# Performance work log

Measured on AMD Instinct MI355X. Metric: run time of the kernel, lower is better.

The kernel has to match this reference:

```python
import jax, jax.numpy as jnp
import numpy as np

B = 4096      # batch
F = 26        # num sparse features
L = 10        # pooling factor (multi-hot indices per feature)
V = 100000    # rows per embedding table
D = 128       # embedding dim (== dense_arch_layer_sizes[-1])
DENSE_IN = 13
DENSE_SIZES = [512, 256, 128]
OVER_SIZES = [1024, 1024, 512, 256, 1]
OVER_IN = D + (F * (F - 1)) // 2 + F  # 479


def _linear_params(key, dims, prefix):
    out = {}
    ks = jax.random.split(key, len(dims) - 1)
    for i in range(len(dims) - 1):
        fan_in = dims[i]
        out[f"{prefix}W{i}"] = jax.random.normal(ks[i], (dims[i], dims[i + 1]), jnp.float32) / np.sqrt(fan_in)
        out[f"{prefix}b{i}"] = jnp.zeros((dims[i + 1],), jnp.float32)
    return out


def setup_inputs() -> dict:
    key = jax.random.key(0)
    k0, k1, k2, k3, k4 = jax.random.split(key, 5)
    inp = {
        "dense_features": jax.random.normal(k0, (B, DENSE_IN), jnp.float32),
        "indices": jax.random.randint(k1, (B, F, L), 0, V, dtype=jnp.int64),
        "tables": jax.random.normal(k2, (F, V, D), jnp.float32) * 0.01,
    }
    inp.update(_linear_params(k3, [DENSE_IN] + DENSE_SIZES, "d"))
    inp.update(_linear_params(k4, [OVER_IN] + OVER_SIZES, "o"))
    return inp


def _dlrm_forward(dense_features, indices, tables,
                  dW0, db0, dW1, db1, dW2, db2,
                  oW0, ob0, oW1, ob1, oW2, ob2, oW3, ob3, oW4, ob4):
    b = dense_features.shape[0]
    # DenseArch: MLP with relu on every layer
    x = dense_features
    for W, bb in ((dW0, db0), (dW1, db1), (dW2, db2)):
        x = jax.nn.relu(x @ W + bb)
    embedded_dense = x  # [B, D]

    # SparseArch: pooled (sum) embedding lookup per feature -> [B, F, D]
    flat_tables = tables.reshape(F * V, D)
    offs = jnp.arange(F, dtype=indices.dtype) * V
    flat_idx = (indices + offs[None, :, None]).reshape(-1)
    gathered = jnp.take(flat_tables, flat_idx, axis=0).reshape(b, F, L, D)
    embedded_sparse = gathered.sum(axis=2)  # [B, F, D]

    # InteractionArch: bmm + upper-triangular gather
    z = jnp.concatenate([embedded_dense[:, None, :], embedded_sparse], axis=1)  # [B, F+1, D]
    inter = jnp.einsum("bnd,bmd->bnm", z, z)  # [B, F+1, F+1]
    iu0, iu1 = np.triu_indices(F + 1, k=1)
    inter_flat = inter[:, iu0, iu1]  # [B, C(F+1,2)]
    feats = jnp.concatenate([embedded_dense, inter_flat], axis=1)  # [B, OVER_IN]

    # OverArch: relu MLP on layer_sizes[:-1], then plain final Linear
    y = feats
    for W, bb in ((oW0, ob0), (oW1, ob1), (oW2, ob2), (oW3, ob3)):
        y = jax.nn.relu(y @ W + bb)
    logits = y @ oW4 + ob4  # [B, 1]
    return logits


def reference(dense_features, indices, tables,
              dW0, db0, dW1, db1, dW2, db2,
              oW0, ob0, oW1, ob1, oW2, ob2, oW3, ob3, oW4, ob4):
    return _dlrm_forward(dense_features, indices, tables,
                         dW0, db0, dW1, db1, dW2, db2,
                         oW0, ob0, oW1, ob1, oW2, ob2, oW3, ob3, oW4, ob4)
```

## Files before the change

kernel.cpp:

```cpp
#include <hip/hip_runtime.h>

#define B_ 4096
#define F_ 26
#define L_ 10
#define V_ 100000
#define D_ 128

typedef __attribute__((ext_vector_type(8))) short short8;
typedef __attribute__((ext_vector_type(4))) float f32x4;

__device__ inline unsigned pack_split(float f) {
    union { float f; unsigned u; } a; a.f = f;
    unsigned r = (a.u + 0x7FFFu + ((a.u >> 16) & 1u)) >> 16;
    union { unsigned u; float f; } hf; hf.u = r << 16;
    float rem = f - hf.f;
    union { float f; unsigned u; } b; b.f = rem;
    unsigned r2 = (b.u + 0x7FFFu + ((b.u >> 16) & 1u)) >> 16;
    return (r << 16) | (r2 & 0xFFFFu);
}
__device__ inline float unpack_f(unsigned u) {
    union { unsigned u; float f; } h; h.u = u & 0xFFFF0000u;
    union { unsigned u; float f; } l; l.u = u << 16;
    return h.f + l.f;
}

__device__ void prep_tile(const float* __restrict__ W, unsigned* __restrict__ Wt,
                          int K, int N, int Kp, int local)
{
    __shared__ float tile[32][33];
    const int t = threadIdx.x;
    const int tx = t & 31, ty = t >> 5;
    const int nbt = N >> 5;
    const int nb = (local % nbt) << 5, kb = (local / nbt) << 5;
    #pragma unroll
    for (int i = 0; i < 4; ++i) {
        int k = kb + ty + i * 8;
        tile[ty + i * 8][tx] = (k < K) ? W[(size_t)k * N + nb + tx] : 0.f;
    }
    __syncthreads();
    #pragma unroll
    for (int i = 0; i < 4; ++i) {
        int nl = ty + i * 8;
        Wt[(size_t)(nb + nl) * Kp + kb + tx] = pack_split(tile[tx][nl]);
    }
}

__global__ __launch_bounds__(256) void prep_all(
    const float* dW0, const float* dW1, const float* dW2,
    const float* oW0, const float* oW1, const float* oW2, const float* oW3,
    unsigned* dWt0, unsigned* dWt1, unsigned* dWt2,
    unsigned* oWt0, unsigned* oWt1, unsigned* oWt2, unsigned* oWt3,
    const float* dense, unsigned* densep)
{
    const int bid = blockIdx.x;
    if      (bid < 16)   prep_tile(dW0, dWt0, 13,   512,  32,   bid);
    else if (bid < 144)  prep_tile(dW1, dWt1, 512,  256,  512,  bid - 16);
    else if (bid < 176)  prep_tile(dW2, dWt2, 256,  128,  256,  bid - 144);
    else if (bid < 656)  prep_tile(oW0, oWt0, 479,  1024, 480,  bid - 176);
    else if (bid < 1680) prep_tile(oW1, oWt1, 1024, 1024, 1024, bid - 656);
    else if (bid < 2192) prep_tile(oW2, oWt2, 1024, 512,  1024, bid - 1680);
    else if (bid < 2320) prep_tile(oW3, oWt3, 512,  256,  512,  bid - 2192);
    else {
        int g = (bid - 2320) * 256 + threadIdx.x;
        int b = g >> 5, k = g & 31;
        densep[g] = (k < 13) ? pack_split(dense[(size_t)b * 13 + k]) : 0u;
    }
}

template<bool RELU>
__global__ __launch_bounds__(256) void gemm_db(
    const unsigned* __restrict__ Ap, const unsigned* __restrict__ Wt,
    const float* __restrict__ bias, unsigned* __restrict__ Cp,
    int M, int N, int Kp)
{
    __shared__ __align__(16) unsigned Au[2][128 * 32];
    __shared__ __align__(16) unsigned Bu[2][128 * 32];

    const int t    = threadIdx.x;
    const int lane = t & 63;
    const int w    = t >> 6;
    const int wm   = w >> 1, wn = w & 1;
    const int m0   = blockIdx.y * 128, n0 = blockIdx.x * 128;

    f32x4 acc[4][4];
    const f32x4 zero = {0.f, 0.f, 0.f, 0.f};
    #pragma unroll
    for (int i = 0; i < 4; ++i)
        #pragma unroll
        for (int j = 0; j < 4; ++j) acc[i][j] = zero;

    const unsigned* Ab = Ap + (size_t)m0 * Kp;
    const unsigned* Bb = Wt + (size_t)n0 * Kp;

    const int g4 = lane >> 4;
    const int rr = lane & 15;

    auto STAGE = [&](int buf, int k0) {
        #pragma unroll
        for (int i = 0; i < 4; ++i) {
            int chunk = t + (i << 8);
            int row = chunk >> 3, ch = chunk & 7;
            int sch = ch ^ (row & 7);
            __builtin_amdgcn_global_load_lds(
                (const __attribute__((address_space(1))) unsigned*)(Ab + (size_t)row * Kp + k0 + (sch << 2)),
                &Au[buf][chunk << 2], 16, 0, 0);
            __builtin_amdgcn_global_load_lds(
                (const __attribute__((address_space(1))) unsigned*)(Bb + (size_t)row * Kp + k0 + (sch << 2)),
                &Bu[buf][chunk << 2], 16, 0, 0);
        }
    };

    auto COMPUTE = [&](int buf) {
        const unsigned* au = Au[buf];
        const unsigned* bu = Bu[buf];
        short8 bh[4], bl[4];
        #pragma unroll
        for (int tj = 0; tj < 4; ++tj) {
            int r = wn * 64 + tj * 16 + rr;
            int c0 = (2 * g4) ^ (r & 7), c1 = (2 * g4 + 1) ^ (r & 7);
            uint4 p = *reinterpret_cast<const uint4*>(&bu[r * 32 + (c0 << 2)]);
            uint4 q = *reinterpret_cast<const uint4*>(&bu[r * 32 + (c1 << 2)]);
            union { short8 s; uint4 u; } H, L;
            H.u.x = __builtin_amdgcn_perm(p.y, p.x, 0x07060302u);
            L.u.x = __builtin_amdgcn_perm(p.y, p.x, 0x05040100u);
            H.u.y = __builtin_amdgcn_perm(p.w, p.z, 0x07060302u);
            L.u.y = __builtin_amdgcn_perm(p.w, p.z, 0x05040100u);
            H.u.z = __builtin_amdgcn_perm(q.y, q.x, 0x07060302u);
            L.u.z = __builtin_amdgcn_perm(q.y, q.x, 0x05040100u);
            H.u.w = __builtin_amdgcn_perm(q.w, q.z, 0x07060302u);
            L.u.w = __builtin_amdgcn_perm(q.w, q.z, 0x05040100u);
            bh[tj] = H.s; bl[tj] = L.s;
        }
        #pragma unroll
        for (int ti = 0; ti < 4; ++ti) {
            int r = wm * 64 + ti * 16 + rr;
            int c0 = (2 * g4) ^ (r & 7), c1 = (2 * g4 + 1) ^ (r & 7);
            uint4 p = *reinterpret_cast<const uint4*>(&au[r * 32 + (c0 << 2)]);
            uint4 q = *reinterpret_cast<const uint4*>(&au[r * 32 + (c1 << 2)]);
            union { short8 s; uint4 u; } H, L;
            H.u.x = __builtin_amdgcn_perm(p.y, p.x, 0x07060302u);
            L.u.x = __builtin_amdgcn_perm(p.y, p.x, 0x05040100u);
            H.u.y = __builtin_amdgcn_perm(p.w, p.z, 0x07060302u);
            L.u.y = __builtin_amdgcn_perm(p.w, p.z, 0x05040100u);
            H.u.z = __builtin_amdgcn_perm(q.y, q.x, 0x07060302u);
            L.u.z = __builtin_amdgcn_perm(q.y, q.x, 0x05040100u);
            H.u.w = __builtin_amdgcn_perm(q.w, q.z, 0x07060302u);
            L.u.w = __builtin_amdgcn_perm(q.w, q.z, 0x05040100u);
            short8 ah = H.s, al = L.s;
            #pragma unroll
            for (int tj = 0; tj < 4; ++tj) {
                f32x4 c = acc[ti][tj];
                c = __builtin_amdgcn_mfma_f32_16x16x32_bf16(ah, bh[tj], c, 0, 0, 0);
                c = __builtin_amdgcn_mfma_f32_16x16x32_bf16(ah, bl[tj], c, 0, 0, 0);
                c = __builtin_amdgcn_mfma_f32_16x16x32_bf16(al, bh[tj], c, 0, 0, 0);
                acc[ti][tj] = c;
            }
        }
    };

    const int nt = Kp >> 5;
    STAGE(0, 0);
    __syncthreads();
    int cur = 0;
    for (int ts = 0; ts < nt - 1; ++ts) {
        STAGE(cur ^ 1, (ts + 1) << 5);
        COMPUTE(cur);
        __syncthreads();
        cur ^= 1;
    }
    COMPUTE(cur);

    #pragma unroll
    for (int ti = 0; ti < 4; ++ti) {
        int row = m0 + wm * 64 + ti * 16 + ((lane >> 4) << 2);
        #pragma unroll
        for (int tj = 0; tj < 4; ++tj) {
            int col = n0 + wn * 64 + tj * 16 + (lane & 15);
            float bv = bias[col];
            #pragma unroll
            for (int r = 0; r < 4; ++r) {
                float v = acc[ti][tj][r] + bv;
                if (RELU) v = fmaxf(v, 0.f);
                Cp[(size_t)(row + r) * N + col] = pack_split(v);
            }
        }
    }
}

__global__ __launch_bounds__(256) void gather_interact(
    const unsigned* __restrict__ x2p,
    const int*      __restrict__ idx_words,
    const float*    __restrict__ tables,
    unsigned*       __restrict__ featsp)
{
    __shared__ __align__(16) float z[27][132];
    __shared__ int sidx[F_ * L_];
    __shared__ int sstride;
    const int b = blockIdx.x;
    const int t = threadIdx.x;

    if (t == 0) {
        int st = 2;
        for (int ww = 1; ww < 256; ww += 2)
            if (idx_words[ww] != 0) { st = 1; break; }
        sstride = st;
        featsp[(size_t)b * 480 + 479] = 0u;
    }
    __syncthreads();
    const int st = sstride;

    for (int s = t; s < F_ * L_; s += 256) {
        int v = idx_words[((size_t)b * F_ * L_ + s) * st];
        sidx[s] = v < 0 ? 0 : (v >= V_ ? V_ - 1 : v);
    }
    if (t < 128) {
        unsigned u = x2p[(size_t)b * 128 + t];
        z[0][t] = unpack_f(u);
        featsp[(size_t)b * 480 + t] = u;
    }
    __syncthreads();

    for (int s = t; s < F_ * 32; s += 256) {
        int f = s >> 5, d4 = s & 31;
        const float* tab = tables + (size_t)f * V_ * D_;
        float4 a4 = {0.f, 0.f, 0.f, 0.f};
        #pragma unroll
        for (int l = 0; l < L_; ++l) {
            int idx = sidx[f * L_ + l];
            float4 v = *reinterpret_cast<const float4*>(tab + (size_t)idx * D_ + (d4 << 2));
            a4.x += v.x; a4.y += v.y; a4.z += v.z; a4.w += v.w;
        }
        *reinterpret_cast<float4*>(&z[f + 1][d4 << 2]) = a4;
    }
    __syncthreads();

    for (int p = t; p < 351; p += 256) {
        int i = 0, rem = p;
        while (rem >= 26 - i) { rem -= 26 - i; ++i; }
        int j = i + 1 + rem;
        float4 s4 = {0.f, 0.f, 0.f, 0.f};
        for (int kk = 0; kk < 32; ++kk) {
            int k4 = (kk + t) & 31;
            float4 a = *reinterpret_cast<const float4*>(&z[i][k4 << 2]);
            float4 c = *reinterpret_cast<const float4*>(&z[j][k4 << 2]);
            s4.x += a.x * c.x; s4.y += a.y * c.y; s4.z += a.z * c.z; s4.w += a.w * c.w;
        }
        featsp[(size_t)b * 480 + 128 + p] = pack_split(s4.x + s4.y + s4.z + s4.w);
    }
}

__global__ __launch_bounds__(256) void final_dot(
    const unsigned* __restrict__ yp, const float* __restrict__ w,
    const float* __restrict__ bias, float* __restrict__ out)
{
    const int wave = threadIdx.x >> 6;
    const int lane = threadIdx.x & 63;
    const int b = blockIdx.x * 4 + wave;
    uint4 u = *reinterpret_cast<const uint4*>(yp + (size_t)b * 256 + lane * 4);
    float4 wv = *reinterpret_cast<const float4*>(&w[lane * 4]);
    float s = unpack_f(u.x) * wv.x + unpack_f(u.y) * wv.y +
              unpack_f(u.z) * wv.z + unpack_f(u.w) * wv.w;
    #pragma unroll
    for (int off = 32; off; off >>= 1) s += __shfl_xor(s, off);
    if (lane == 0) out[b] = s + bias[0];
}

extern "C" void kernel_launch(void* const* d_in, const int* in_sizes, int n_in,
                              void* d_out, int out_size, void* d_ws, size_t ws_size,
                              hipStream_t stream)
{
    const float* dense   = (const float*)d_in[0];
    const int*   indices = (const int*)  d_in[1];
    const float* tables  = (const float*)d_in[2];
    const float* dW0 = (const float*)d_in[3];  const float* db0 = (const float*)d_in[4];
    const float* dW1 = (const float*)d_in[5];  const float* db1 = (const float*)d_in[6];
    const float* dW2 = (const float*)d_in[7];  const float* db2 = (const float*)d_in[8];
    const float* oW0 = (const float*)d_in[9];  const float* ob0 = (const float*)d_in[10];
    const float* oW1 = (const float*)d_in[11]; const float* ob1 = (const float*)d_in[12];
    const float* oW2 = (const float*)d_in[13]; const float* ob2 = (const float*)d_in[14];
    const float* oW3 = (const float*)d_in[15]; const float* ob3 = (const float*)d_in[16];
    const float* oW4 = (const float*)d_in[17]; const float* ob4 = (const float*)d_in[18];
    float* out = (float*)d_out;

    unsigned* wsu = (unsigned*)d_ws;
    unsigned* dWt0 = wsu + 0;
    unsigned* dWt1 = wsu + 16384;
    unsigned* dWt2 = wsu + 147456;
    unsigned* oWt0 = wsu + 180224;
    unsigned* oWt1 = wsu + 671744;
    unsigned* oWt2 = wsu + 1720320;
    unsigned* oWt3 = wsu + 2244608;
    unsigned* densep = wsu + 2375680;
    unsigned* x2p    = wsu + 2506752;
    unsigned* featsp = wsu + 3031040;
    unsigned* x0p    = wsu + 5000000;
    unsigned* x1p    = wsu + 7097152;
    unsigned* y0p    = wsu + 5000000;
    unsigned* y1p    = wsu + 9194304;
    unsigned* y2p    = wsu + 2506752;
    unsigned* y3p    = wsu + 5000000;

    prep_all<<<2832, 256, 0, stream>>>(dW0, dW1, dW2, oW0, oW1, oW2, oW3,
                                       dWt0, dWt1, dWt2, oWt0, oWt1, oWt2, oWt3,
                                       dense, densep);

    gemm_db<true><<<dim3(4, B_ / 128), 256, 0, stream>>>(densep, dWt0, db0, x0p, B_, 512, 32);
    gemm_db<true><<<dim3(2, B_ / 128), 256, 0, stream>>>(x0p,    dWt1, db1, x1p, B_, 256, 512);
    gemm_db<true><<<dim3(1, B_ / 128), 256, 0, stream>>>(x1p,    dWt2, db2, x2p, B_, 128, 256);

    gather_interact<<<B_, 256, 0, stream>>>(x2p, indices, tables, featsp);

    gemm_db<true><<<dim3(8, B_ / 128), 256, 0, stream>>>(featsp, oWt0, ob0, y0p, B_, 1024, 480);
    gemm_db<true><<<dim3(8, B_ / 128), 256, 0, stream>>>(y0p,    oWt1, ob1, y1p, B_, 1024, 1024);
    gemm_db<true><<<dim3(4, B_ / 128), 256, 0, stream>>>(y1p,    oWt2, ob2, y2p, B_, 512, 1024);
    gemm_db<true><<<dim3(2, B_ / 128), 256, 0, stream>>>(y2p,    oWt3, ob3, y3p, B_, 256, 512);

    final_dot<<<B_ / 4, 256, 0, stream>>>(y3p, oW4, ob4, out);
}
```

Baseline: 327.2 us.

## Use 8-wave GEMM blocks and MFMA-based per-sample interaction with wave-per-sample gather

The GEMM kernel now runs 512 threads (8 waves) per 128x128 tile, so each wave owns a 64x32 sub-tile and keeps fewer accumulators, which is meant to raise latency hiding without changing the tile size. The embedding gather and interaction kernel is restructured so each wave handles one sample. The pooled embeddings are split into bf16 hi/lo halves in swizzled LDS, and the 27x27 Gram matrix is computed with split-bf16 MFMA instead of scalar float dot products. This removes the scalar triangular loop and shrinks the grid, at the cost of computing the full padded 32x32 product and using fewer threads per gather.

```diff
diff --git a/kernel.cpp b/kernel.cpp
--- a/kernel.cpp
+++ b/kernel.cpp
@@ -68,7 +68,7 @@
 }
 
 template<bool RELU>
-__global__ __launch_bounds__(256) void gemm_db(
+__global__ __launch_bounds__(512) void gemm8(
     const unsigned* __restrict__ Ap, const unsigned* __restrict__ Wt,
     const float* __restrict__ bias, unsigned* __restrict__ Cp,
     int M, int N, int Kp)
@@ -79,15 +79,15 @@
     const int t    = threadIdx.x;
     const int lane = t & 63;
     const int w    = t >> 6;
-    const int wm   = w >> 1, wn = w & 1;
+    const int wm   = w >> 2, wn = w & 3;
     const int m0   = blockIdx.y * 128, n0 = blockIdx.x * 128;
 
-    f32x4 acc[4][4];
+    f32x4 acc[4][2];
     const f32x4 zero = {0.f, 0.f, 0.f, 0.f};
     #pragma unroll
     for (int i = 0; i < 4; ++i)
         #pragma unroll
-        for (int j = 0; j < 4; ++j) acc[i][j] = zero;
+        for (int j = 0; j < 2; ++j) acc[i][j] = zero;
 
     const unsigned* Ab = Ap + (size_t)m0 * Kp;
     const unsigned* Bb = Wt + (size_t)n0 * Kp;
@@ -97,13 +97,19 @@
 
     auto STAGE = [&](int buf, int k0) {
         #pragma unroll
-        for (int i = 0; i < 4; ++i) {
-            int chunk = t + (i << 8);
+        for (int i = 0; i < 2; ++i) {
+            int chunk = t + (i << 9);
             int row = chunk >> 3, ch = chunk & 7;
             int sch = ch ^ (row & 7);
             __builtin_amdgcn_global_load_lds(
                 (const __attribute__((address_space(1))) unsigned*)(Ab + (size_t)row * Kp + k0 + (sch << 2)),
                 &Au[buf][chunk << 2], 16, 0, 0);
+        }
+        #pragma unroll
+        for (int i = 0; i < 2; ++i) {
+            int chunk = t + (i << 9);
+            int row = chunk >> 3, ch = chunk & 7;
+            int sch = ch ^ (row & 7);
             __builtin_amdgcn_global_load_lds(
                 (const __attribute__((address_space(1))) unsigned*)(Bb + (size_t)row * Kp + k0 + (sch << 2)),
                 &Bu[buf][chunk << 2], 16, 0, 0);
@@ -113,10 +119,10 @@
     auto COMPUTE = [&](int buf) {
         const unsigned* au = Au[buf];
         const unsigned* bu = Bu[buf];
-        short8 bh[4], bl[4];
-        #pragma unroll
-        for (int tj = 0; tj < 4; ++tj) {
-            int r = wn * 64 + tj * 16 + rr;
+        short8 bh[2], bl[2];
+        #pragma unroll
+        for (int tj = 0; tj < 2; ++tj) {
+            int r = wn * 32 + tj * 16 + rr;
             int c0 = (2 * g4) ^ (r & 7), c1 = (2 * g4 + 1) ^ (r & 7);
             uint4 p = *reinterpret_cast<const uint4*>(&bu[r * 32 + (c0 << 2)]);
             uint4 q = *reinterpret_cast<const uint4*>(&bu[r * 32 + (c1 << 2)]);
@@ -148,7 +154,7 @@
             L.u.w = __builtin_amdgcn_perm(q.w, q.z, 0x05040100u);
             short8 ah = H.s, al = L.s;
             #pragma unroll
-            for (int tj = 0; tj < 4; ++tj) {
+            for (int tj = 0; tj < 2; ++tj) {
                 f32x4 c = acc[ti][tj];
                 c = __builtin_amdgcn_mfma_f32_16x16x32_bf16(ah, bh[tj], c, 0, 0, 0);
                 c = __builtin_amdgcn_mfma_f32_16x16x32_bf16(ah, bl[tj], c, 0, 0, 0);
@@ -172,10 +178,10 @@
 
     #pragma unroll
     for (int ti = 0; ti < 4; ++ti) {
-        int row = m0 + wm * 64 + ti * 16 + ((lane >> 4) << 2);
-        #pragma unroll
-        for (int tj = 0; tj < 4; ++tj) {
-            int col = n0 + wn * 64 + tj * 16 + (lane & 15);
+        int row = m0 + wm * 64 + ti * 16 + (g4 << 2);
+        #pragma unroll
+        for (int tj = 0; tj < 2; ++tj) {
+            int col = n0 + wn * 32 + tj * 16 + rr;
             float bv = bias[col];
             #pragma unroll
             for (int r = 0; r < 4; ++r) {
@@ -187,65 +193,101 @@
     }
 }
 
-__global__ __launch_bounds__(256) void gather_interact(
+__global__ __launch_bounds__(256) void gather_interact_mfma(
     const unsigned* __restrict__ x2p,
     const int*      __restrict__ idx_words,
     const float*    __restrict__ tables,
     unsigned*       __restrict__ featsp)
 {
-    __shared__ __align__(16) float z[27][132];
-    __shared__ int sidx[F_ * L_];
+    __shared__ unsigned zh[4][32][64];
+    __shared__ unsigned zl[4][32][64];
+    __shared__ int sidx[4][F_ * L_];
     __shared__ int sstride;
-    const int b = blockIdx.x;
-    const int t = threadIdx.x;
+
+    const int t    = threadIdx.x;
+    const int w    = t >> 6;
+    const int lane = t & 63;
+    const int s    = blockIdx.x * 4 + w;
 
     if (t == 0) {
         int st = 2;
         for (int ww = 1; ww < 256; ww += 2)
             if (idx_words[ww] != 0) { st = 1; break; }
         sstride = st;
-        featsp[(size_t)b * 480 + 479] = 0u;
     }
     __syncthreads();
     const int st = sstride;
 
-    for (int s = t; s < F_ * L_; s += 256) {
-        int v = idx_words[((size_t)b * F_ * L_ + s) * st];
-        sidx[s] = v < 0 ? 0 : (v >= V_ ? V_ - 1 : v);
-    }
-    if (t < 128) {
-        unsigned u = x2p[(size_t)b * 128 + t];
-        z[0][t] = unpack_f(u);
-        featsp[(size_t)b * 480 + t] = u;
-    }
-    __syncthreads();
-
-    for (int s = t; s < F_ * 32; s += 256) {
-        int f = s >> 5, d4 = s & 31;
+    for (int q = lane; q < F_ * L_; q += 64) {
+        int v = idx_words[((size_t)s * F_ * L_ + q) * st];
+        sidx[w][q] = v < 0 ? 0 : (v >= V_ ? V_ - 1 : v);
+    }
+    uint2 xv = *reinterpret_cast<const uint2*>(x2p + (size_t)s * 128 + 2 * lane);
+    *reinterpret_cast<uint2*>(featsp + (size_t)s * 480 + 2 * lane) = xv;
+    if (lane == 0) featsp[(size_t)s * 480 + 479] = 0u;
+    zh[w][0][lane] = (xv.x >> 16) | (xv.y & 0xFFFF0000u);
+    zl[w][0][lane] = (xv.x & 0xFFFFu) | (xv.y << 16);
+    __syncthreads();
+
+    for (int f = 0; f < F_; ++f) {
+        float2 a = {0.f, 0.f};
         const float* tab = tables + (size_t)f * V_ * D_;
-        float4 a4 = {0.f, 0.f, 0.f, 0.f};
         #pragma unroll
         for (int l = 0; l < L_; ++l) {
-            int idx = sidx[f * L_ + l];
-            float4 v = *reinterpret_cast<const float4*>(tab + (size_t)idx * D_ + (d4 << 2));
-            a4.x += v.x; a4.y += v.y; a4.z += v.z; a4.w += v.w;
-        }
-        *reinterpret_cast<float4*>(&z[f + 1][d4 << 2]) = a4;
-    }
-    __syncthreads();
-
-    for (int p = t; p < 351; p += 256) {
-        int i = 0, rem = p;
-        while (rem >= 26 - i) { rem -= 26 - i; ++i; }
-        int j = i + 1 + rem;
-        float4 s4 = {0.f, 0.f, 0.f, 0.f};
-        for (int kk = 0; kk < 32; ++kk) {
-            int k4 = (kk + t) & 31;
-            float4 a = *reinterpret_cast<const float4*>(&z[i][k4 << 2]);
-            float4 c = *reinterpret_cast<const float4*>(&z[j][k4 << 2]);
-            s4.x += a.x * c.x; s4.y += a.y * c.y; s4.z += a.z * c.z; s4.w += a.w * c.w;
-        }
-        featsp[(size_t)b * 480 + 128 + p] = pack_split(s4.x + s4.y + s4.z + s4.w);
+            int idx = sidx[w][f * L_ + l];
+            float2 v = *reinterpret_cast<const float2*>(tab + (size_t)idx * D_ + 2 * lane);
+            a.x += v.x; a.y += v.y;
+        }
+        unsigned px = pack_split(a.x), py = pack_split(a.y);
+        int r  = f + 1;
+        int dw = (((lane >> 2) ^ (r & 7)) << 2) + (lane & 3);
+        zh[w][r][dw] = (px >> 16) | (py & 0xFFFF0000u);
+        zl[w][r][dw] = (px & 0xFFFFu) | (py << 16);
+    }
+    __syncthreads();
+
+    const int g4 = lane >> 4;
+    const int rr = lane & 15;
+    f32x4 acc[2][2];
+    const f32x4 zero = {0.f, 0.f, 0.f, 0.f};
+    acc[0][0] = zero; acc[0][1] = zero; acc[1][0] = zero; acc[1][1] = zero;
+
+    #pragma unroll
+    for (int ks = 0; ks < 4; ++ks) {
+        short8 h[2], lo[2];
+        #pragma unroll
+        for (int mi = 0; mi < 2; ++mi) {
+            int r = mi * 16 + rr;
+            int c = (ks * 4 + g4) ^ (r & 7);
+            h[mi]  = *reinterpret_cast<const short8*>(&zh[w][r][c << 2]);
+            lo[mi] = *reinterpret_cast<const short8*>(&zl[w][r][c << 2]);
+        }
+        #pragma unroll
+        for (int mi = 0; mi < 2; ++mi)
+            #pragma unroll
+            for (int nj = 0; nj < 2; ++nj) {
+                f32x4 c = acc[mi][nj];
+                c = __builtin_amdgcn_mfma_f32_16x16x32_bf16(h[mi],  h[nj],  c, 0, 0, 0);
+                c = __builtin_amdgcn_mfma_f32_16x16x32_bf16(h[mi],  lo[nj], c, 0, 0, 0);
+                c = __builtin_amdgcn_mfma_f32_16x16x32_bf16(lo[mi], h[nj],  c, 0, 0, 0);
+                acc[mi][nj] = c;
+            }
+    }
+
+    #pragma unroll
+    for (int mi = 0; mi < 2; ++mi) {
+        #pragma unroll
+        for (int nj = 0; nj < 2; ++nj) {
+            #pragma unroll
+            for (int r = 0; r < 4; ++r) {
+                int i = mi * 16 + g4 * 4 + r;
+                int j = nj * 16 + rr;
+                if (i < j && j <= 26) {
+                    int p = i * 26 - (i * (i - 1)) / 2 + (j - i - 1);
+                    featsp[(size_t)s * 480 + 128 + p] = pack_split(acc[mi][nj][r]);
+                }
+            }
+        }
     }
 }
 
@@ -304,16 +346,16 @@
                                        dWt0, dWt1, dWt2, oWt0, oWt1, oWt2, oWt3,
                                        dense, densep);
 
-    gemm_db<true><<<dim3(4, B_ / 128), 256, 0, stream>>>(densep, dWt0, db0, x0p, B_, 512, 32);
-    gemm_db<true><<<dim3(2, B_ / 128), 256, 0, stream>>>(x0p,    dWt1, db1, x1p, B_, 256, 512);
-    gemm_db<true><<<dim3(1, B_ / 128), 256, 0, stream>>>(x1p,    dWt2, db2, x2p, B_, 128, 256);
-
-    gather_interact<<<B_, 256, 0, stream>>>(x2p, indices, tables, featsp);
-
-    gemm_db<true><<<dim3(8, B_ / 128), 256, 0, stream>>>(featsp, oWt0, ob0, y0p, B_, 1024, 480);
-    gemm_db<true><<<dim3(8, B_ / 128), 256, 0, stream>>>(y0p,    oWt1, ob1, y1p, B_, 1024, 1024);
-    gemm_db<true><<<dim3(4, B_ / 128), 256, 0, stream>>>(y1p,    oWt2, ob2, y2p, B_, 512, 1024);
-    gemm_db<true><<<dim3(2, B_ / 128), 256, 0, stream>>>(y2p,    oWt3, ob3, y3p, B_, 256, 512);
+    gemm8<true><<<dim3(4, B_ / 128), 512, 0, stream>>>(densep, dWt0, db0, x0p, B_, 512, 32);
+    gemm8<true><<<dim3(2, B_ / 128), 512, 0, stream>>>(x0p,    dWt1, db1, x1p, B_, 256, 512);
+    gemm8<true><<<dim3(1, B_ / 128), 512, 0, stream>>>(x1p,    dWt2, db2, x2p, B_, 128, 256);
+
+    gather_interact_mfma<<<B_ / 4, 256, 0, stream>>>(x2p, indices, tables, featsp);
+
+    gemm8<true><<<dim3(8, B_ / 128), 512, 0, stream>>>(featsp, oWt0, ob0, y0p, B_, 1024, 480);
+    gemm8<true><<<dim3(8, B_ / 128), 512, 0, stream>>>(y0p,    oWt1, ob1, y1p, B_, 1024, 1024);
+    gemm8<true><<<dim3(4, B_ / 128), 512, 0, stream>>>(y1p,    oWt2, ob2, y2p, B_, 512, 1024);
+    gemm8<true><<<dim3(2, B_ / 128), 512, 0, stream>>>(y2p,    oWt3, ob3, y3p, B_, 256, 512);
 
     final_dot<<<B_ / 4, 256, 0, stream>>>(y3p, oW4, ob4, out);
 }
```

Result: faster. 294.6 us (-10.0%).
